# Kernel optimization log

Measured on AMD Instinct MI355X. Metric: run time of the kernel, lower is better.

## Reference

```python
import jax, jax.numpy as jnp
from jax import lax
import numpy as np

DN = ('NCHW', 'OIHW', 'NCHW')
PAD = [(1, 1), (1, 1)]  # padding=1 each side
STRIDE = (1, 1)


def setup_inputs() -> dict:
    key = jax.random.key(0)
    k0, k1, k2, k3, k4, k5 = jax.random.split(key, 6)
    B, Cin, Cout, H, W, K, FES = 32, 96, 144, 56, 56, 3, 3
    fan_main = Cin * K * K
    fan_extra = FES * K * K
    x = jax.random.normal(k0, (B, Cin, H, W), dtype=jnp.float32)
    extra_inputs = jax.random.normal(k1, (B, Cout * FES), dtype=jnp.float32)
    Wm = jax.random.normal(k2, (Cout, Cin, K, K), dtype=jnp.float32) / np.sqrt(fan_main)
    bm = jax.random.normal(k3, (Cout,), dtype=jnp.float32) * 0.01
    Wx = jax.random.normal(k4, (Cout, FES, K, K), dtype=jnp.float32) / np.sqrt(fan_extra)
    bx = jax.random.normal(k5, (Cout,), dtype=jnp.float32) * 0.01
    return {"x": x, "extra_inputs": extra_inputs, "Wm": Wm, "bm": bm, "Wx": Wx, "bx": bx}


def reference(x, extra_inputs, Wm, bm, Wx, bx):
    # main path: standard conv + bias
    main = lax.conv_general_dilated(x, Wm, STRIDE, PAD, dimension_numbers=DN)
    main = main + bm[None, :, None, None]

    B = x.shape[0]
    Cout, FES, kh, kw = Wx.shape
    H2, W2 = main.shape[2], main.shape[3]

    # Extra path: each extra conv operates on a spatially-constant map, so
    # conv(const_c) = const_c * conv(ones). Compute per-(out,fes)-kernel response
    # to a ones map once (captures zero-padding boundary effects exactly),
    # then combine via a batched einsum — collapsing the per-channel loop.
    ones = jnp.ones((1, 1, x.shape[2], x.shape[3]), dtype=x.dtype)
    M = lax.conv_general_dilated(
        ones, Wx.reshape(Cout * FES, 1, kh, kw), STRIDE, PAD, dimension_numbers=DN
    )  # [1, Cout*FES, H2, W2]
    M = M.reshape(Cout, FES, H2, W2)

    extra = extra_inputs.reshape(B, Cout, FES)
    extra_out = jnp.einsum('bif,ifhw->bihw', extra, M) + bx[None, :, None, None]

    return main + extra_out
```

## Files before the change

kernel.cpp:

```cpp
#include <hip/hip_runtime.h>
#include <hip/hip_bf16.h>

#define B_    32
#define CIN   96
#define COUT  144
#define H_    56
#define W_    56
#define HW    3136
#define NPIX  100352
#define KTOT  864
#define MT    256
#define TAPSZ (COUT*CIN)

typedef short  short8  __attribute__((ext_vector_type(8)));
typedef float  floatx4 __attribute__((ext_vector_type(4)));

__device__ __attribute__((aligned(64))) float g_zero[64];

__device__ __forceinline__ unsigned short f2bf(float f) {
    union { float f; unsigned int u; } v; v.f = f;
    unsigned int u = v.u;
    return (unsigned short)((u + 0x7FFFu + ((u >> 16) & 1u)) >> 16);
}

__device__ __forceinline__ void glds16(const void* g, void* l) {
    __builtin_amdgcn_global_load_lds(
        (const __attribute__((address_space(1))) unsigned int*)g,
        (__attribute__((address_space(3))) unsigned int*)l, 16, 0, 0);
}

#define TB 1568
#define WB 486
__global__ __launch_bounds__(256) void prep_all(const float* __restrict__ x,
                                                unsigned short* __restrict__ xT,
                                                const float* __restrict__ Wm,
                                                unsigned short* __restrict__ Wt,
                                                const float* __restrict__ extra,
                                                const float* __restrict__ Wx,
                                                const float* __restrict__ bm,
                                                const float* __restrict__ bx,
                                                float* __restrict__ E) {
    __shared__ __align__(16) unsigned short tile[64][CIN + 8];
    int blk = blockIdx.x;
    int t = threadIdx.x;
    if (blk < TB) {
        int b   = blk / 49;
        int hw0 = (blk % 49) * 64;
        const float* xb = x + (size_t)b * CIN * HW;
        for (int i = t; i < CIN * 16; i += 256) {
            int ci = i >> 4, seg = i & 15;
            float4 v = *(const float4*)(xb + (size_t)ci * HW + hw0 + seg * 4);
            int hwl = seg * 4;
            tile[hwl + 0][ci] = f2bf(v.x);
            tile[hwl + 1][ci] = f2bf(v.y);
            tile[hwl + 2][ci] = f2bf(v.z);
            tile[hwl + 3][ci] = f2bf(v.w);
        }
        __syncthreads();
        int row = t >> 2, part = t & 3;
        const uint4* s = (const uint4*)&tile[row][part * 24];
        uint4* d = (uint4*)(xT + ((size_t)b * HW + hw0 + row) * CIN + part * 24);
        d[0] = s[0]; d[1] = s[1]; d[2] = s[2];
    } else if (blk < TB + WB) {
        int i = (blk - TB) * 256 + t;
        int tap = i / TAPSZ;
        int rem = i - tap * TAPSZ;
        int co  = rem / CIN, ci = rem - co * CIN;
        Wt[i] = f2bf(Wm[((size_t)co * CIN + ci) * 9 + tap]);
    } else {
        int i = (blk - TB - WB) * 256 + t;
        int b = i / COUT, co = i - b * COUT;
        float base = bm[co] + bx[co];
        float m[3][3] = {{0,0,0},{0,0,0},{0,0,0}};
        for (int f = 0; f < 3; ++f) {
            float e = extra[(size_t)b * (COUT * 3) + co * 3 + f];
            const float* w = Wx + ((size_t)co * 3 + f) * 9;
            for (int rc = 0; rc < 3; ++rc) {
                int kh0 = (rc == 0) ? 1 : 0;
                int kh1 = (rc == 2) ? 1 : 2;
                for (int cc = 0; cc < 3; ++cc) {
                    int kw0 = (cc == 0) ? 1 : 0;
                    int kw1 = (cc == 2) ? 1 : 2;
                    float s = 0.f;
                    for (int kh = kh0; kh <= kh1; ++kh)
                        for (int kw = kw0; kw <= kw1; ++kw)
                            s += w[kh * 3 + kw];
                    m[rc][cc] += e * s;
                }
            }
        }
        float* dst = E + (size_t)i * 9;
        for (int rc = 0; rc < 3; ++rc)
            for (int cc = 0; cc < 3; ++cc)
                dst[rc * 3 + cc] = base + m[rc][cc];
    }
}

__global__ __launch_bounds__(256, 1) void conv_gemm(const unsigned short* __restrict__ xT,
                                                    const unsigned short* __restrict__ Wt,
                                                    const float* __restrict__ E,
                                                    float* __restrict__ out) {
    __shared__ __align__(16) unsigned short Bs[2 * TAPSZ];

    int tid = threadIdx.x;
    int wv = tid >> 6, lane = tid & 63;
    int r16 = lane & 15, q = lane >> 4;
    int pixBase = blockIdx.x * MT;

    floatx4 acc[4][9];
    #pragma unroll
    for (int m = 0; m < 4; ++m)
        #pragma unroll
        for (int n = 0; n < 9; ++n)
            acc[m][n] = (floatx4){0.f, 0.f, 0.f, 0.f};

    int aIdx[4], hA[4], wA[4];
    #pragma unroll
    for (int ms = 0; ms < 4; ++ms) {
        int p = pixBase + wv * 64 + ms * 16 + r16;
        aIdx[ms] = p * CIN;
        int hw = p % HW;
        hA[ms] = hw / W_;
        wA[ms] = hw - hA[ms] * W_;
    }
    const unsigned short* gz = (const unsigned short*)g_zero;

    int bSrc[7];
    #pragma unroll
    for (int j = 0; j < 7; ++j) {
        int s = tid + j * 256;
        int g = s / COUT, co = s - g * COUT;
        bSrc[j] = co * CIN + g * 8;
    }
    const bool bTail = (tid < 192);

    const unsigned short* BpBase = Bs + (q * COUT + r16) * 8;

    short8 a[2][4][3];

    {
        const unsigned short* wsrc = Wt;
        #pragma unroll
        for (int j = 0; j < 6; ++j)
            glds16(wsrc + bSrc[j], (void*)(Bs + tid * 8 + j * 2048));
        if (bTail)
            glds16(wsrc + bSrc[6], (void*)(Bs + tid * 8 + 6 * 2048));
        const int dh = -1, dw = -1, off = (dh * W_ + dw) * CIN;
        #pragma unroll
        for (int ms = 0; ms < 4; ++ms) {
            bool valid = ((unsigned)(hA[ms] + dh) < H_) && ((unsigned)(wA[ms] + dw) < W_);
            const unsigned short* base = valid ? (xT + aIdx[ms] + off) : gz;
            #pragma unroll
            for (int ks = 0; ks < 3; ++ks)
                a[0][ms][ks] = *(const short8*)(base + ks * 32 + q * 8);
        }
    }
    __syncthreads();

    #pragma unroll
    for (int tap = 0; tap < 9; ++tap) {
        const int cur = tap & 1, nxt = cur ^ 1;

        if (tap < 8) {
            const int tap2 = tap + 1;
            const int dh2 = tap2 / 3 - 1, dw2 = tap2 - (tap2 / 3) * 3 - 1;
            const unsigned short* wsrc = Wt + tap2 * TAPSZ;
            unsigned short* bd = Bs + nxt * TAPSZ;
            #pragma unroll
            for (int j = 0; j < 6; ++j)
                glds16(wsrc + bSrc[j], (void*)(bd + tid * 8 + j * 2048));
            if (bTail)
                glds16(wsrc + bSrc[6], (void*)(bd + tid * 8 + 6 * 2048));
            const int off2 = (dh2 * W_ + dw2) * CIN;
            #pragma unroll
            for (int ms = 0; ms < 4; ++ms) {
                bool valid = ((unsigned)(hA[ms] + dh2) < H_) && ((unsigned)(wA[ms] + dw2) < W_);
                const unsigned short* base = valid ? (xT + aIdx[ms] + off2) : gz;
                #pragma unroll
                for (int ks = 0; ks < 3; ++ks)
                    a[nxt][ms][ks] = *(const short8*)(base + ks * 32 + q * 8);
            }
        }

        const unsigned short* Bp = BpBase + cur * TAPSZ;
        #pragma unroll
        for (int ks = 0; ks < 3; ++ks) {
            short8 bf[9];
            #pragma unroll
            for (int n = 0; n < 9; ++n)
                bf[n] = *(const short8*)(Bp + ks * 4608 + n * 128);
            #pragma unroll
            for (int n = 0; n < 9; ++n)
                #pragma unroll
                for (int ms = 0; ms < 4; ++ms)
                    acc[ms][n] = __builtin_amdgcn_mfma_f32_16x16x32_bf16(
                        a[cur][ms][ks], bf[n], acc[ms][n], 0, 0, 0);
        }

        __syncthreads();
    }

    #pragma unroll
    for (int ms = 0; ms < 4; ++ms) {
        int p0 = pixBase + wv * 64 + ms * 16 + q * 4;
        int b  = p0 / HW;
        int hw0 = p0 - b * HW;
        int h = hw0 / W_;
        int w0 = hw0 - h * W_;
        int rc = (h == 0) ? 0 : ((h == H_ - 1) ? 2 : 1);
        int cc0 = (w0 == 0) ? 0 : ((w0 == W_ - 1) ? 2 : 1);
        int cc1 = (w0 + 1 == W_ - 1) ? 2 : 1;
        int cc2 = (w0 + 2 == W_ - 1) ? 2 : 1;
        int cc3 = (w0 + 3 == W_ - 1) ? 2 : 1;
        const float* Ebase = E + (size_t)b * COUT * 9 + rc * 3;
        float* outB = out + (size_t)b * COUT * HW + hw0;
        #pragma unroll
        for (int n = 0; n < 9; ++n) {
            int co = n * 16 + r16;
            const float* Eb = Ebase + co * 9;
            float4 v;
            v.x = acc[ms][n][0] + Eb[cc0];
            v.y = acc[ms][n][1] + Eb[cc1];
            v.z = acc[ms][n][2] + Eb[cc2];
            v.w = acc[ms][n][3] + Eb[cc3];
            *(float4*)(outB + (size_t)co * HW) = v;
        }
    }
}

extern "C" void kernel_launch(void* const* d_in, const int* in_sizes, int n_in,
                              void* d_out, int out_size, void* d_ws, size_t ws_size,
                              hipStream_t stream) {
    const float* x     = (const float*)d_in[0];
    const float* extra = (const float*)d_in[1];
    const float* Wm    = (const float*)d_in[2];
    const float* bm    = (const float*)d_in[3];
    const float* Wx    = (const float*)d_in[4];
    const float* bx    = (const float*)d_in[5];
    float* out = (float*)d_out;

    const size_t XT_BYTES = (size_t)NPIX * CIN * 2;
    const size_t WT_BYTES = (size_t)COUT * KTOT * 2;
    const size_t E_BYTES  = (size_t)B_ * COUT * 9 * 4;
    if (ws_size < XT_BYTES + WT_BYTES + E_BYTES) return;

    unsigned short* xT = (unsigned short*)d_ws;
    unsigned short* Wt = (unsigned short*)((char*)d_ws + XT_BYTES);
    float*          E  = (float*)((char*)d_ws + XT_BYTES + WT_BYTES);

    prep_all<<<TB + WB + 18, 256, 0, stream>>>(x, xT, Wm, Wt, extra, Wx, bm, bx, E);
    conv_gemm<<<NPIX / MT, 256, 0, stream>>>(xT, Wt, E, out);
}
```

Before: 159.8 us.

## Regroup activations and weights into MFMA fragment layout, split A prefetch per k-slice

The prep kernel now writes activations into 16-pixel groups laid out to match the MFMA fragment order (k-slice, quad, row), and weights with channel groups of 8 contiguous per output channel. This lets each lane's A and B loads hit contiguous 16-byte chunks instead of a stride of CIN. The GEMM loop refills each k-slice's A registers right after that slice is consumed, which cuts live A registers from 24 to 16 short8s. It also sets launch_bounds to 2 blocks per CU, but the LDS double buffer is about 55KB, so occupancy may not actually rise and the tighter register cap could cause spills.

```diff
diff --git a/kernel.cpp b/kernel.cpp
--- a/kernel.cpp
+++ b/kernel.cpp
@@ -11,11 +11,12 @@
 #define KTOT  864
 #define MT    256
 #define TAPSZ (COUT*CIN)
+#define GRP   1536
 
 typedef short  short8  __attribute__((ext_vector_type(8)));
 typedef float  floatx4 __attribute__((ext_vector_type(4)));
 
-__device__ __attribute__((aligned(64))) float g_zero[64];
+__device__ __attribute__((aligned(64))) float g_zero[16];
 
 __device__ __forceinline__ unsigned short f2bf(float f) {
     union { float f; unsigned int u; } v; v.f = f;
@@ -32,9 +33,9 @@
 #define TB 1568
 #define WB 486
 __global__ __launch_bounds__(256) void prep_all(const float* __restrict__ x,
-                                                unsigned short* __restrict__ xT,
+                                                unsigned short* __restrict__ xA,
                                                 const float* __restrict__ Wm,
-                                                unsigned short* __restrict__ Wt,
+                                                unsigned short* __restrict__ Wt2,
                                                 const float* __restrict__ extra,
                                                 const float* __restrict__ Wx,
                                                 const float* __restrict__ bm,
@@ -57,16 +58,28 @@
             tile[hwl + 3][ci] = f2bf(v.w);
         }
         __syncthreads();
-        int row = t >> 2, part = t & 3;
-        const uint4* s = (const uint4*)&tile[row][part * 24];
-        uint4* d = (uint4*)(xT + ((size_t)b * HW + hw0 + row) * CIN + part * 24);
-        d[0] = s[0]; d[1] = s[1]; d[2] = s[2];
+        int g0 = (b * HW + hw0) >> 4;
+        #pragma unroll
+        for (int jj = 0; jj < 3; ++jj) {
+            int c = t + jj * 256;
+            int r = c & 15;
+            int y = c >> 4;
+            int qq = y & 3;
+            int z = y >> 2;
+            int ks = z % 3, tl = z / 3;
+            const uint4* s = (const uint4*)&tile[tl * 16 + r][ks * 32 + qq * 8];
+            uint4* d = (uint4*)(xA + (size_t)(g0 + tl) * GRP + ks * 512 + qq * 128 + r * 8);
+            *d = *s;
+        }
     } else if (blk < TB + WB) {
         int i = (blk - TB) * 256 + t;
         int tap = i / TAPSZ;
         int rem = i - tap * TAPSZ;
-        int co  = rem / CIN, ci = rem - co * CIN;
-        Wt[i] = f2bf(Wm[((size_t)co * CIN + ci) * 9 + tap]);
+        int g   = rem / (COUT * 8);
+        int rr  = rem - g * (COUT * 8);
+        int co  = rr >> 3, j = rr & 7;
+        int ci  = g * 8 + j;
+        Wt2[i] = f2bf(Wm[((size_t)co * CIN + ci) * 9 + tap]);
     } else {
         int i = (blk - TB - WB) * 256 + t;
         int b = i / COUT, co = i - b * COUT;
@@ -96,8 +109,8 @@
     }
 }
 
-__global__ __launch_bounds__(256, 1) void conv_gemm(const unsigned short* __restrict__ xT,
-                                                    const unsigned short* __restrict__ Wt,
+__global__ __launch_bounds__(256, 2) void conv_gemm(const unsigned short* __restrict__ xA,
+                                                    const unsigned short* __restrict__ Wt2,
                                                     const float* __restrict__ E,
                                                     float* __restrict__ out) {
     __shared__ __align__(16) unsigned short Bs[2 * TAPSZ];
@@ -114,11 +127,11 @@
         for (int n = 0; n < 9; ++n)
             acc[m][n] = (floatx4){0.f, 0.f, 0.f, 0.f};
 
-    int aIdx[4], hA[4], wA[4];
+    int pms[4], hA[4], wA[4];
     #pragma unroll
     for (int ms = 0; ms < 4; ++ms) {
         int p = pixBase + wv * 64 + ms * 16 + r16;
-        aIdx[ms] = p * CIN;
+        pms[ms] = p;
         int hw = p % HW;
         hA[ms] = hw / W_;
         wA[ms] = hw - hA[ms] * W_;
@@ -130,71 +143,95 @@
     for (int j = 0; j < 7; ++j) {
         int s = tid + j * 256;
         int g = s / COUT, co = s - g * COUT;
-        bSrc[j] = co * CIN + g * 8;
+        bSrc[j] = g * (COUT * 8) + co * 8;
     }
     const bool bTail = (tid < 192);
 
     const unsigned short* BpBase = Bs + (q * COUT + r16) * 8;
 
-    short8 a[2][4][3];
-
-    {
-        const unsigned short* wsrc = Wt;
-        #pragma unroll
-        for (int j = 0; j < 6; ++j)
-            glds16(wsrc + bSrc[j], (void*)(Bs + tid * 8 + j * 2048));
-        if (bTail)
-            glds16(wsrc + bSrc[6], (void*)(Bs + tid * 8 + 6 * 2048));
-        const int dh = -1, dw = -1, off = (dh * W_ + dw) * CIN;
-        #pragma unroll
-        for (int ms = 0; ms < 4; ++ms) {
-            bool valid = ((unsigned)(hA[ms] + dh) < H_) && ((unsigned)(wA[ms] + dw) < W_);
-            const unsigned short* base = valid ? (xT + aIdx[ms] + off) : gz;
-            #pragma unroll
-            for (int ks = 0; ks < 3; ++ks)
-                a[0][ms][ks] = *(const short8*)(base + ks * 32 + q * 8);
-        }
+    short8 a01[4][2];
+    short8 a2[2][4];
+
+#define ALOAD(dst, ms, ks, dh, dw, off)                                         \
+    {                                                                           \
+        int p_ = pms[ms] + (off);                                               \
+        bool v_ = ((unsigned)(hA[ms] + (dh)) < H_) &&                           \
+                  ((unsigned)(wA[ms] + (dw)) < W_);                             \
+        const unsigned short* ptr_ = v_                                         \
+            ? (xA + (long)(p_ >> 4) * GRP + (p_ & 15) * 8 + q * 128 + (ks) * 512)\
+            : gz;                                                               \
+        dst = *(const short8*)ptr_;                                             \
+    }
+
+#define STAGE_B(tap_, bd_)                                                      \
+    {                                                                           \
+        const unsigned short* wsrc_ = Wt2 + (tap_) * TAPSZ;                     \
+        _Pragma("unroll")                                                       \
+        for (int j = 0; j < 6; ++j)                                             \
+            glds16(wsrc_ + bSrc[j], (void*)((bd_) + tid * 8 + j * 2048));       \
+        if (bTail)                                                              \
+            glds16(wsrc_ + bSrc[6], (void*)((bd_) + tid * 8 + 6 * 2048));       \
+    }
+
+    STAGE_B(0, Bs);
+    #pragma unroll
+    for (int ms = 0; ms < 4; ++ms) {
+        ALOAD(a01[ms][0], ms, 0, -1, -1, -57);
+        ALOAD(a01[ms][1], ms, 1, -1, -1, -57);
+        ALOAD(a2[0][ms],  ms, 2, -1, -1, -57);
     }
     __syncthreads();
 
     #pragma unroll
     for (int tap = 0; tap < 9; ++tap) {
         const int cur = tap & 1, nxt = cur ^ 1;
+        const int tap2 = tap + 1;
+        const int dh2 = tap2 / 3 - 1, dw2 = tap2 - (tap2 / 3) * 3 - 1;
+        const int off2 = dh2 * W_ + dw2;
+        const unsigned short* Bp = BpBase + cur * TAPSZ;
 
         if (tap < 8) {
-            const int tap2 = tap + 1;
-            const int dh2 = tap2 / 3 - 1, dw2 = tap2 - (tap2 / 3) * 3 - 1;
-            const unsigned short* wsrc = Wt + tap2 * TAPSZ;
-            unsigned short* bd = Bs + nxt * TAPSZ;
-            #pragma unroll
-            for (int j = 0; j < 6; ++j)
-                glds16(wsrc + bSrc[j], (void*)(bd + tid * 8 + j * 2048));
-            if (bTail)
-                glds16(wsrc + bSrc[6], (void*)(bd + tid * 8 + 6 * 2048));
-            const int off2 = (dh2 * W_ + dw2) * CIN;
-            #pragma unroll
-            for (int ms = 0; ms < 4; ++ms) {
-                bool valid = ((unsigned)(hA[ms] + dh2) < H_) && ((unsigned)(wA[ms] + dw2) < W_);
-                const unsigned short* base = valid ? (xT + aIdx[ms] + off2) : gz;
-                #pragma unroll
-                for (int ks = 0; ks < 3; ++ks)
-                    a[nxt][ms][ks] = *(const short8*)(base + ks * 32 + q * 8);
-            }
-        }
-
-        const unsigned short* Bp = BpBase + cur * TAPSZ;
-        #pragma unroll
-        for (int ks = 0; ks < 3; ++ks) {
-            short8 bf[9];
-            #pragma unroll
-            for (int n = 0; n < 9; ++n)
-                bf[n] = *(const short8*)(Bp + ks * 4608 + n * 128);
-            #pragma unroll
-            for (int n = 0; n < 9; ++n)
-                #pragma unroll
-                for (int ms = 0; ms < 4; ++ms)
-                    acc[ms][n] = __builtin_amdgcn_mfma_f32_16x16x32_bf16(
-                        a[cur][ms][ks], bf[n], acc[ms][n], 0, 0, 0);
+            STAGE_B(tap2, Bs + nxt * TAPSZ);
+            #pragma unroll
+            for (int ms = 0; ms < 4; ++ms)
+                ALOAD(a2[nxt][ms], ms, 2, dh2, dw2, off2);
+        }
+
+        #pragma unroll
+        for (int n = 0; n < 9; ++n) {
+            short8 bfv = *(const short8*)(Bp + n * 128);
+            #pragma unroll
+            for (int ms = 0; ms < 4; ++ms)
+                acc[ms][n] = __builtin_amdgcn_mfma_f32_16x16x32_bf16(
+                    a01[ms][0], bfv, acc[ms][n], 0, 0, 0);
+        }
+        if (tap < 8) {
+            #pragma unroll
+            for (int ms = 0; ms < 4; ++ms)
+                ALOAD(a01[ms][0], ms, 0, dh2, dw2, off2);
+        }
+
+        #pragma unroll
+        for (int n = 0; n < 9; ++n) {
+            short8 bfv = *(const short8*)(Bp + 4608 + n * 128);
+            #pragma unroll
+            for (int ms = 0; ms < 4; ++ms)
+                acc[ms][n] = __builtin_amdgcn_mfma_f32_16x16x32_bf16(
+                    a01[ms][1], bfv, acc[ms][n], 0, 0, 0);
+        }
+        if (tap < 8) {
+            #pragma unroll
+            for (int ms = 0; ms < 4; ++ms)
+                ALOAD(a01[ms][1], ms, 1, dh2, dw2, off2);
+        }
+
+        #pragma unroll
+        for (int n = 0; n < 9; ++n) {
+            short8 bfv = *(const short8*)(Bp + 2 * 4608 + n * 128);
+            #pragma unroll
+            for (int ms = 0; ms < 4; ++ms)
+                acc[ms][n] = __builtin_amdgcn_mfma_f32_16x16x32_bf16(
+                    a2[cur][ms], bfv, acc[ms][n], 0, 0, 0);
         }
 
         __syncthreads();
@@ -226,6 +263,8 @@
             *(float4*)(outB + (size_t)co * HW) = v;
         }
     }
+#undef ALOAD
+#undef STAGE_B
 }
 
 extern "C" void kernel_launch(void* const* d_in, const int* in_sizes, int n_in,
@@ -239,15 +278,15 @@
     const float* bx    = (const float*)d_in[5];
     float* out = (float*)d_out;
 
-    const size_t XT_BYTES = (size_t)NPIX * CIN * 2;
+    const size_t XA_BYTES = (size_t)NPIX * CIN * 2;
     const size_t WT_BYTES = (size_t)COUT * KTOT * 2;
     const size_t E_BYTES  = (size_t)B_ * COUT * 9 * 4;
-    if (ws_size < XT_BYTES + WT_BYTES + E_BYTES) return;
-
-    unsigned short* xT = (unsigned short*)d_ws;
-    unsigned short* Wt = (unsigned short*)((char*)d_ws + XT_BYTES);
-    float*          E  = (float*)((char*)d_ws + XT_BYTES + WT_BYTES);
-
-    prep_all<<<TB + WB + 18, 256, 0, stream>>>(x, xT, Wm, Wt, extra, Wx, bm, bx, E);
-    conv_gemm<<<NPIX / MT, 256, 0, stream>>>(xT, Wt, E, out);
-}
+    if (ws_size < XA_BYTES + WT_BYTES + E_BYTES) return;
+
+    unsigned short* xA  = (unsigned short*)d_ws;
+    unsigned short* Wt2 = (unsigned short*)((char*)d_ws + XA_BYTES);
+    float*          E   = (float*)((char*)d_ws + XA_BYTES + WT_BYTES);
+
+    prep_all<<<TB + WB + 18, 256, 0, stream>>>(x, xA, Wm, Wt2, extra, Wx, bm, bx, E);
+    conv_gemm<<<NPIX / MT, 256, 0, stream>>>(xA, Wt2, E, out);
+}
```

Result: slower. 182.9 us (+14.5%).
